# Kernel tuning notes

Hardware: AMD Instinct MI355X
Metric: run time of the kernel (lower is better)

## Reference

```python
import jax, jax.numpy as jnp
import numpy as np

N_TASK, N_WORKER, N_STATION = 20000, 5000, 1000
D, HEADS, LAYERS = 64, 4, 2
EDGE_COUNTS = [50000, 30000, 30000, 40000, 40000]
# (n_src, n_dst) per relation: precedes, assigned_to, has_task, can_do, done_by
EDGE_SPEC = [(N_TASK, N_TASK), (N_TASK, N_STATION), (N_STATION, N_TASK), (N_WORKER, N_TASK), (N_TASK, N_WORKER)]
EDGE_TYPES = [('task', 'task'), ('task', 'station'), ('station', 'task'), ('worker', 'task'), ('task', 'worker')]


def setup_inputs() -> dict:
    key = jax.random.key(0)
    ks = iter(jax.random.split(key, 64))
    inp = {}
    inp['x_task'] = jax.random.normal(next(ks), (N_TASK, 16), jnp.float32)
    inp['x_worker'] = jax.random.normal(next(ks), (N_WORKER, 12), jnp.float32)
    inp['x_station'] = jax.random.normal(next(ks), (N_STATION, 10), jnp.float32)
    for i, (E, (ns, nd)) in enumerate(zip(EDGE_COUNTS, EDGE_SPEC)):
        src = jax.random.randint(next(ks), (E,), 0, ns)
        dst = jax.random.randint(next(ks), (E,), 0, nd)
        inp[f'ei{i}'] = jnp.stack([src, dst]).astype(jnp.int32)
    def lin(k, i, o):
        return jax.random.normal(k, (i, o), jnp.float32) / np.float32(np.sqrt(i))
    # feature embedder params (Linear + LayerNorm affine) per node type
    for name, fd in [('task', 16), ('worker', 12), ('station', 10)]:
        inp[f'W_{name}'] = lin(next(ks), fd, D)
        inp[f'b_{name}'] = jnp.zeros((D,), jnp.float32)
        inp[f'g_{name}'] = jnp.ones((D,), jnp.float32)
        inp[f'beta_{name}'] = jnp.zeros((D,), jnp.float32)
    # stacked GATv2 params: [layers, 5 edge types, ...]
    inp['gat_Wl'] = jax.random.normal(next(ks), (LAYERS, 5, D, HEADS * D), jnp.float32) / np.float32(np.sqrt(D))
    inp['gat_Wr'] = jax.random.normal(next(ks), (LAYERS, 5, D, HEADS * D), jnp.float32) / np.float32(np.sqrt(D))
    inp['gat_att'] = jax.random.normal(next(ks), (LAYERS, 5, HEADS, D), jnp.float32) * np.float32(0.1)
    inp['gat_bias'] = jnp.zeros((LAYERS, 5, D), jnp.float32)
    return inp


def _layer_norm(x, g, b):
    m = x.mean(-1, keepdims=True)
    v = ((x - m) ** 2).mean(-1, keepdims=True)
    return (x - m) * jax.lax.rsqrt(v + 1e-5) * g + b


def _gatv2(x_src, x_dst, ei, Wl, Wr, att, bias):
    # GATv2Conv, concat=False (mean over heads), no self loops
    n_dst = x_dst.shape[0]
    xl = (x_src @ Wl).reshape(-1, HEADS, D)  # [Ns,H,Dh]
    xr = (x_dst @ Wr).reshape(-1, HEADS, D)  # [Nd,H,Dh]
    src, dst = ei[0], ei[1]
    e = jax.nn.leaky_relu(xl[src] + xr[dst], 0.2)          # [E,H,Dh]
    logits = jnp.einsum('ehd,hd->eh', e, att)              # [E,H]
    m = jax.ops.segment_max(logits, dst, num_segments=n_dst)
    ex = jnp.exp(logits - m[dst])
    denom = jax.ops.segment_sum(ex, dst, num_segments=n_dst)
    alpha = ex / denom[dst]                                # segment softmax per dst node
    out = jax.ops.segment_sum(alpha[..., None] * xl[src], dst, num_segments=n_dst)
    return out.mean(axis=1) + bias                         # [Nd,D]


def _forward(x_task, x_worker, x_station, eis,
             W_task, b_task, g_task, beta_task,
             W_worker, b_worker, g_worker, beta_worker,
             W_station, b_station, g_station, beta_station,
             gat_Wl, gat_Wr, gat_att, gat_bias):
    x = {
        'task': jax.nn.relu(_layer_norm(x_task @ W_task + b_task, g_task, beta_task)),
        'worker': jax.nn.relu(_layer_norm(x_worker @ W_worker + b_worker, g_worker, beta_worker)),
        'station': jax.nn.relu(_layer_norm(x_station @ W_station + b_station, g_station, beta_station)),
    }
    for l in range(LAYERS):
        agg = {'task': 0.0, 'worker': 0.0, 'station': 0.0}
        for t, (st, dt) in enumerate(EDGE_TYPES):
            agg[dt] = agg[dt] + _gatv2(x[st], x[dt], eis[t], gat_Wl[l, t], gat_Wr[l, t], gat_att[l, t], gat_bias[l, t])
        x = {k: jax.nn.relu(agg[k]) + x[k] for k in x}  # HeteroConv sum aggr, then ReLU + residual
    gc = jnp.concatenate([
        x['station'].mean(0), x['task'].mean(0), x['worker'].mean(0),
        x['station'].max(0), x['task'].max(0), x['worker'].max(0),
    ])[None, :]  # [1, 6*D]
    return x['task'], x['worker'], x['station'], gc


def reference(x_task, x_worker, x_station, ei0, ei1, ei2, ei3, ei4,
              W_task, b_task, g_task, beta_task,
              W_worker, b_worker, g_worker, beta_worker,
              W_station, b_station, g_station, beta_station,
              gat_Wl, gat_Wr, gat_att, gat_bias):
    return _forward(x_task, x_worker, x_station, (ei0, ei1, ei2, ei3, ei4),
                    W_task, b_task, g_task, beta_task,
                    W_worker, b_worker, g_worker, beta_worker,
                    W_station, b_station, g_station, beta_station,
                    gat_Wl, gat_Wr, gat_att, gat_bias)
```

## Files before the change

kernel.cpp:

```cpp
#include <hip/hip_runtime.h>
#include <math.h>

#define NT 20000
#define NW 5000
#define NS 1000

typedef __attribute__((ext_vector_type(8))) short bf16x8;
typedef __attribute__((ext_vector_type(4))) float f32x4;

struct GemmSeg { const short* X; const short* Wt; short* Y; int N; int blk0; };
struct GemmTab { GemmSeg s[10]; int nseg; };

struct GatSeg { const int* rowp; const int* col; const short* xl; const short* xr;
                const float* att; const float* bias; float* agg; int Nd; int wave0; };
struct GatTab { GatSeg s[5]; int nseg; };

struct EdgeSeg { const int* ei; int* cnt; int* col; int E; int blk0; };
struct EdgeTab { EdgeSeg s[5]; int nseg; };

struct ScanTab { int* cnt[5]; int* rowp[5]; int n[5]; };

__device__ __forceinline__ float wsum64(float v) {
  #pragma unroll
  for (int o = 32; o > 0; o >>= 1) v += __shfl_xor(v, o, 64);
  return v;
}
__device__ __forceinline__ short f2b(float f) {
  unsigned u = __float_as_uint(f);
  unsigned r = (u + 0x7FFFu + ((u >> 16) & 1u)) >> 16;
  return (short)(unsigned short)r;
}
__device__ __forceinline__ float blo(unsigned x) { return __uint_as_float(x << 16); }
__device__ __forceinline__ float bhi(unsigned x) { return __uint_as_float(x & 0xFFFF0000u); }

__global__ void wprep_kernel(const float* __restrict__ gWl, const float* __restrict__ gWr,
                             short* __restrict__ Wlt, short* __restrict__ Wrt) {
  int idx = blockIdx.x * 256 + threadIdx.x;
  int side = idx >= 163840;
  int j = idx - side * 163840;
  int m = j >> 14;
  int e = j & 16383;
  int k = e >> 8, colv = e & 255;
  const float* src = side ? gWr : gWl;
  short* dst = side ? Wrt : Wlt;
  dst[m * 16384 + colv * 64 + k] = f2b(src[m * 16384 + e]);
}

__global__ void embed_kernel(const float* __restrict__ x, const float* __restrict__ W,
                             const float* __restrict__ b, const float* __restrict__ g,
                             const float* __restrict__ beta, float* __restrict__ y,
                             short* __restrict__ yb, int N, int FD) {
  int gid  = blockIdx.x * blockDim.x + threadIdx.x;
  int wid  = gid >> 6;
  int lane = gid & 63;
  if (wid >= N) return;
  const float* xr = x + (size_t)wid * FD;
  float acc = b[lane];
  for (int k = 0; k < FD; ++k) acc = fmaf(xr[k], W[k * 64 + lane], acc);
  float m = wsum64(acc) * (1.f / 64.f);
  float d = acc - m;
  float v = wsum64(d * d) * (1.f / 64.f);
  float o = d * rsqrtf(v + 1e-5f) * g[lane] + beta[lane];
  o = fmaxf(o, 0.f);
  y[(size_t)wid * 64 + lane] = o;
  yb[(size_t)wid * 64 + lane] = f2b(o);
}

__global__ void zero_kernel(unsigned int* __restrict__ p, long long n) {
  long long i  = (long long)blockIdx.x * blockDim.x + threadIdx.x;
  long long st = (long long)gridDim.x * blockDim.x;
  for (; i < n; i += st) p[i] = 0u;
}

__global__ void count_kernel(EdgeTab tab) {
  int b = blockIdx.x, si = 0;
  for (int i = 1; i < tab.nseg; ++i) if (b >= tab.s[i].blk0) si = i;
  EdgeSeg sg = tab.s[si];
  int e = (b - sg.blk0) * 256 + threadIdx.x;
  if (e < sg.E) atomicAdd(&sg.cnt[sg.ei[sg.E + e]], 1);
}

__global__ void scan_kernel(ScanTab tab) {
  int t = blockIdx.x;
  int* cnt = tab.cnt[t]; int* rowp = tab.rowp[t]; int n = tab.n[t];
  __shared__ int wsums[16];
  __shared__ int carry_s;
  int tid = threadIdx.x, lane = tid & 63, w = tid >> 6;
  if (tid == 0) carry_s = 0;
  __syncthreads();
  for (int base = 0; base < n; base += 1024) {
    int i = base + tid;
    int v = (i < n) ? cnt[i] : 0;
    int s = v;
    #pragma unroll
    for (int o = 1; o < 64; o <<= 1) { int x = __shfl_up(s, o, 64); if (lane >= o) s += x; }
    if (lane == 63) wsums[w] = s;
    __syncthreads();
    if (w == 0 && lane < 16) {
      int x = wsums[lane];
      #pragma unroll
      for (int o = 1; o < 16; o <<= 1) { int y = __shfl_up(x, o, 16); if (lane >= o) x += y; }
      wsums[lane] = x;
    }
    __syncthreads();
    int carry   = carry_s;
    int waveoff = (w == 0) ? 0 : wsums[w - 1];
    int exc     = carry + waveoff + s - v;
    if (i < n) { rowp[i] = exc; cnt[i] = exc; }
    __syncthreads();
    if (tid == 0) carry_s += wsums[15];
    __syncthreads();
  }
  if (threadIdx.x == 0) rowp[n] = carry_s;
}

__global__ void fill_kernel(EdgeTab tab) {
  int b = blockIdx.x, si = 0;
  for (int i = 1; i < tab.nseg; ++i) if (b >= tab.s[i].blk0) si = i;
  EdgeSeg sg = tab.s[si];
  int e = (b - sg.blk0) * 256 + threadIdx.x;
  if (e >= sg.E) return;
  int s = sg.ei[e], d = sg.ei[sg.E + e];
  int pos = atomicAdd(&sg.cnt[d], 1);
  sg.col[pos] = s;
}

__global__ __launch_bounds__(256) void gemm_kernel(GemmTab tab) {
  __shared__ short lds[4096 + 16384];
  int b = blockIdx.x, si = 0;
  for (int i = 1; i < tab.nseg; ++i) if (b >= tab.s[i].blk0) si = i;
  GemmSeg sg = tab.s[si];
  int r0 = (b - sg.blk0) * 64;
  int tid = threadIdx.x;
  #pragma unroll
  for (int it = 0; it < 2; ++it) {
    int idx = it * 256 + tid;
    int row = idx >> 3, kq = idx & 7;
    bf16x8 v = {0, 0, 0, 0, 0, 0, 0, 0};
    if (r0 + row < sg.N) v = *(const bf16x8*)&sg.X[(size_t)(r0 + row) * 64 + kq * 8];
    *(bf16x8*)&lds[(row * 8 + (kq ^ (row & 7))) * 8] = v;
  }
  #pragma unroll
  for (int it = 0; it < 8; ++it) {
    int idx = it * 256 + tid;
    int col = idx >> 3, kq = idx & 7;
    bf16x8 v = *(const bf16x8*)&sg.Wt[col * 64 + kq * 8];
    *(bf16x8*)&lds[4096 + (col * 8 + (kq ^ (col & 7))) * 8] = v;
  }
  __syncthreads();
  int lane = tid & 63, wv = tid >> 6;
  int r = lane & 15, hk = lane >> 4;
  f32x4 acc[4][4];
  #pragma unroll
  for (int rt = 0; rt < 4; ++rt)
    #pragma unroll
    for (int ct = 0; ct < 4; ++ct) acc[rt][ct] = (f32x4){0.f, 0.f, 0.f, 0.f};
  #pragma unroll
  for (int kk = 0; kk < 2; ++kk) {
    int kq = kk * 4 + hk;
    bf16x8 a[4], bb[4];
    #pragma unroll
    for (int rt = 0; rt < 4; ++rt) {
      int row = rt * 16 + r;
      a[rt] = *(const bf16x8*)&lds[(row * 8 + (kq ^ (row & 7))) * 8];
    }
    #pragma unroll
    for (int ct = 0; ct < 4; ++ct) {
      int col = wv * 64 + ct * 16 + r;
      bb[ct] = *(const bf16x8*)&lds[4096 + (col * 8 + (kq ^ (col & 7))) * 8];
    }
    #pragma unroll
    for (int rt = 0; rt < 4; ++rt)
      #pragma unroll
      for (int ct = 0; ct < 4; ++ct)
        acc[rt][ct] = __builtin_amdgcn_mfma_f32_16x16x32_bf16(a[rt], bb[ct], acc[rt][ct], 0, 0, 0);
  }
  #pragma unroll
  for (int rt = 0; rt < 4; ++rt) {
    #pragma unroll
    for (int j = 0; j < 4; ++j) {
      int row = r0 + rt * 16 + hk * 4 + j;
      if (row < sg.N) {
        #pragma unroll
        for (int ct = 0; ct < 4; ++ct) {
          int col = wv * 64 + ct * 16 + r;
          sg.Y[(size_t)row * 256 + col] = f2b(acc[rt][ct][j]);
        }
      }
    }
  }
}

__global__ void gat_kernel(GatTab tab) {
  int gwave = (blockIdx.x * blockDim.x + threadIdx.x) >> 6;
  int lane  = threadIdx.x & 63;
  int si = 0;
  for (int i = 1; i < tab.nseg; ++i) if (gwave >= tab.s[i].wave0) si = i;
  GatSeg sg = tab.s[si];
  int n = gwave - sg.wave0;
  if (n >= sg.Nd) return;
  int h = lane >> 4, lig = lane & 15;
  int beg = sg.rowp[n], end = sg.rowp[n + 1];
  uint2 xru = *(const uint2*)&sg.xr[(size_t)n * 256 + h * 64 + lig * 4];
  float xr0 = blo(xru.x), xr1 = bhi(xru.x), xr2 = blo(xru.y), xr3 = bhi(xru.y);
  float4 a4 = *(const float4*)&sg.att[h * 64 + lig * 4];
  float den = 0.f, c0 = 0.f, c1 = 0.f, c2 = 0.f, c3 = 0.f;
  if (end > beg) {
    int sNxt = sg.col[beg];
    uint2 w = *(const uint2*)&sg.xl[(size_t)sNxt * 256 + h * 64 + lig * 4];
    if (beg + 1 < end) sNxt = sg.col[beg + 1];
    for (int i = beg; i < end; ++i) {
      uint2 wc = w;
      if (i + 1 < end)
        w = *(const uint2*)&sg.xl[(size_t)sNxt * 256 + h * 64 + lig * 4];
      if (i + 2 < end) sNxt = sg.col[i + 2];
      float f0 = blo(wc.x), f1 = bhi(wc.x), f2v = blo(wc.y), f3 = bhi(wc.y);
      float vx = f0 + xr0, vy = f1 + xr1, vz = f2v + xr2, vw = f3 + xr3;
      vx = fmaxf(vx, 0.2f * vx); vy = fmaxf(vy, 0.2f * vy);
      vz = fmaxf(vz, 0.2f * vz); vw = fmaxf(vw, 0.2f * vw);
      float d = fmaf(vx, a4.x, fmaf(vy, a4.y, fmaf(vz, a4.z, vw * a4.w)));
      d += __shfl_xor(d, 1, 64);
      d += __shfl_xor(d, 2, 64);
      d += __shfl_xor(d, 4, 64);
      d += __shfl_xor(d, 8, 64);
      float e = __expf(d);
      den += e;
      c0 = fmaf(e, f0, c0); c1 = fmaf(e, f1, c1);
      c2 = fmaf(e, f2v, c2); c3 = fmaf(e, f3, c3);
    }
  }
  float4 o = make_float4(0.f, 0.f, 0.f, 0.f);
  if (end > beg) {
    float inv = 1.f / den;
    o.x = c0 * inv; o.y = c1 * inv; o.z = c2 * inv; o.w = c3 * inv;
  }
  o.x += __shfl_xor(o.x, 16, 64); o.x += __shfl_xor(o.x, 32, 64);
  o.y += __shfl_xor(o.y, 16, 64); o.y += __shfl_xor(o.y, 32, 64);
  o.z += __shfl_xor(o.z, 16, 64); o.z += __shfl_xor(o.z, 32, 64);
  o.w += __shfl_xor(o.w, 16, 64); o.w += __shfl_xor(o.w, 32, 64);
  if (lane < 16) {
    float4 b4 = *(const float4*)&sg.bias[lane * 4];
    float4 res;
    res.x = fmaf(0.25f, o.x, b4.x); res.y = fmaf(0.25f, o.y, b4.y);
    res.z = fmaf(0.25f, o.z, b4.z); res.w = fmaf(0.25f, o.w, b4.w);
    *(float4*)&sg.agg[(size_t)n * 64 + lane * 4] = res;
  }
}

__global__ void combine_kernel(const float* __restrict__ aT0, const float* __restrict__ aT2,
                               const float* __restrict__ aT3, const float* __restrict__ aW,
                               const float* __restrict__ aS,
                               const float* __restrict__ xT, const float* __restrict__ xW,
                               const float* __restrict__ xS,
                               float* __restrict__ oT, float* __restrict__ oW,
                               float* __restrict__ oS,
                               short* __restrict__ bT, short* __restrict__ bW,
                               short* __restrict__ bS) {
  int i = blockIdx.x * 256 + threadIdx.x;
  const int nT = NT * 64, nW = NW * 64, nS = NS * 64;
  if (i < nT) {
    float v = fmaxf(aT0[i] + aT2[i] + aT3[i], 0.f) + xT[i];
    oT[i] = v; if (bT) bT[i] = f2b(v);
  } else if (i < nT + nW) {
    int j = i - nT;
    float v = fmaxf(aW[j], 0.f) + xW[j];
    oW[j] = v; if (bW) bW[j] = f2b(v);
  } else if (i < nT + nW + nS) {
    int j = i - nT - nW;
    float v = fmaxf(aS[j], 0.f) + xS[j];
    oS[j] = v; if (bS) bS[j] = f2b(v);
  }
}

__global__ __launch_bounds__(256) void pool1_kernel(const float* __restrict__ xt,
                                                    const float* __restrict__ xw,
                                                    const float* __restrict__ xs,
                                                    float* __restrict__ part_sum,
                                                    float* __restrict__ part_max) {
  int b = blockIdx.x;
  const float* x; int N, base, nb;
  if (b < 80)       { x = xt; N = NT; base = 0;   nb = 80; }
  else if (b < 100) { x = xw; N = NW; base = 80;  nb = 20; }
  else              { x = xs; N = NS; base = 100; nb = 4;  }
  int local = b - base;
  int lane = threadIdx.x & 63, w = threadIdx.x >> 6;
  int waveIdx = local * 4 + w, stride = nb * 4;
  float s = 0.f, mx = -3e38f;
  for (int r = waveIdx; r < N; r += stride) {
    float v = x[(size_t)r * 64 + lane];
    s += v; mx = fmaxf(mx, v);
  }
  __shared__ float ss[4][64], sm[4][64];
  ss[w][lane] = s; sm[w][lane] = mx;
  __syncthreads();
  if (w == 0) {
    #pragma unroll
    for (int i = 1; i < 4; ++i) { s += ss[i][lane]; mx = fmaxf(mx, sm[i][lane]); }
    part_sum[(size_t)b * 64 + lane] = s;
    part_max[(size_t)b * 64 + lane] = mx;
  }
}

__global__ void pool2_kernel(const float* __restrict__ part_sum,
                             const float* __restrict__ part_max,
                             float* __restrict__ gc) {
  int b = blockIdx.x;
  int lane = threadIdx.x & 63, w = threadIdx.x >> 6;
  int off, cnt, N, mi;
  if (b == 0)      { off = 100; cnt = 4;  N = NS; mi = 0;   }
  else if (b == 1) { off = 0;   cnt = 80; N = NT; mi = 64;  }
  else             { off = 80;  cnt = 20; N = NW; mi = 128; }
  float s = 0.f, mx = -3e38f;
  for (int i = w; i < cnt; i += 4) {
    s += part_sum[(size_t)(off + i) * 64 + lane];
    mx = fmaxf(mx, part_max[(size_t)(off + i) * 64 + lane]);
  }
  __shared__ float ss[4][64], sm[4][64];
  ss[w][lane] = s; sm[w][lane] = mx;
  __syncthreads();
  if (w == 0) {
    #pragma unroll
    for (int i = 1; i < 4; ++i) { s += ss[i][lane]; mx = fmaxf(mx, sm[i][lane]); }
    gc[mi + lane] = s / (float)N;
    gc[192 + mi + lane] = mx;
  }
}

extern "C" void kernel_launch(void* const* d_in, const int* in_sizes, int n_in,
                              void* d_out, int out_size, void* d_ws, size_t ws_size,
                              hipStream_t stream) {
  const float* x_in[3] = {(const float*)d_in[0], (const float*)d_in[1], (const float*)d_in[2]};
  const int*   ei[5]   = {(const int*)d_in[3], (const int*)d_in[4], (const int*)d_in[5],
                          (const int*)d_in[6], (const int*)d_in[7]};
  const float* Wemb[3] = {(const float*)d_in[8],  (const float*)d_in[12], (const float*)d_in[16]};
  const float* bemb[3] = {(const float*)d_in[9],  (const float*)d_in[13], (const float*)d_in[17]};
  const float* gemb[3] = {(const float*)d_in[10], (const float*)d_in[14], (const float*)d_in[18]};
  const float* beemb[3]= {(const float*)d_in[11], (const float*)d_in[15], (const float*)d_in[19]};
  const float* gWl   = (const float*)d_in[20];
  const float* gWr   = (const float*)d_in[21];
  const float* gatt  = (const float*)d_in[22];
  const float* gbias = (const float*)d_in[23];

  const int NN[3]  = {NT, NW, NS};
  const int FD[3]  = {16, 12, 10};
  const int EC[5]  = {50000, 30000, 30000, 40000, 40000};
  const int STy[5] = {0, 0, 2, 1, 0};
  const int DTy[5] = {0, 2, 0, 0, 1};

  char* p = (char*)d_ws;
  auto alloc = [&](size_t bytes) -> void* {
    void* r = (void*)p;
    p += (bytes + 255) & ~(size_t)255;
    return r;
  };
  float* xc[3];  short* xcb[3];
  for (int k = 0; k < 3; ++k) xc[k]  = (float*)alloc((size_t)NN[k] * 64 * 4);
  for (int k = 0; k < 3; ++k) xcb[k] = (short*)alloc((size_t)NN[k] * 64 * 2);
  float* aggT0 = (float*)alloc((size_t)NT * 64 * 4);
  float* aggS  = (float*)alloc((size_t)NS * 64 * 4);
  float* aggT2 = (float*)alloc((size_t)NT * 64 * 4);
  float* aggT3 = (float*)alloc((size_t)NT * 64 * 4);
  float* aggW  = (float*)alloc((size_t)NW * 64 * 4);
  float* aggOf[5] = {aggT0, aggS, aggT2, aggT3, aggW};
  int* nxtAll = (int*)alloc((size_t)66000 * 4);
  int  nxtOff[5] = {0, NT, NT + NS, 2 * NT + NS, 3 * NT + NS};
  int* nxt[5]; for (int t = 0; t < 5; ++t) nxt[t] = nxtAll + nxtOff[t];
  int *rowp[5], *col[5];
  for (int t = 0; t < 5; ++t) {
    rowp[t] = (int*)alloc((size_t)(NN[DTy[t]] + 1) * 4);
    col[t]  = (int*)alloc((size_t)EC[t] * 4);
  }
  float* psum = (float*)alloc((size_t)104 * 64 * 4);
  float* pmax = (float*)alloc((size_t)104 * 64 * 4);
  short* Wlt  = (short*)alloc((size_t)10 * 16384 * 2);
  short* Wrt  = (short*)alloc((size_t)10 * 16384 * 2);

  size_t used = (size_t)(p - (char*)d_ws);
  size_t fusedExtra = (size_t)132000 * 256 * 2 + (1 << 20);
  bool fused = (ws_size - used) >= fusedExtra;
  short *xlT[5], *xrT[5];
  if (fused) {
    for (int t = 0; t < 5; ++t) {
      xlT[t] = (short*)alloc((size_t)NN[STy[t]] * 256 * 2);
      xrT[t] = (short*)alloc((size_t)NN[DTy[t]] * 256 * 2);
    }
  } else {
    short* xlb = (short*)alloc((size_t)NT * 256 * 2);
    short* xrb = (short*)alloc((size_t)NT * 256 * 2);
    for (int t = 0; t < 5; ++t) { xlT[t] = xlb; xrT[t] = xrb; }
  }

  wprep_kernel<<<1280, 256, 0, stream>>>(gWl, gWr, Wlt, Wrt);

  for (int k = 0; k < 3; ++k) {
    int threads = NN[k] * 64;
    embed_kernel<<<(threads + 255) / 256, 256, 0, stream>>>(
        x_in[k], Wemb[k], bemb[k], gemb[k], beemb[k], xc[k], xcb[k], NN[k], FD[k]);
  }

  zero_kernel<<<64, 256, 0, stream>>>((unsigned*)nxtAll, 66000);
  EdgeTab etab; etab.nseg = 5;
  int eb = 0;
  for (int t = 0; t < 5; ++t) {
    etab.s[t] = {ei[t], nxt[t], col[t], EC[t], eb};
    eb += (EC[t] + 255) / 256;
  }
  count_kernel<<<eb, 256, 0, stream>>>(etab);
  ScanTab stab;
  for (int t = 0; t < 5; ++t) { stab.cnt[t] = nxt[t]; stab.rowp[t] = rowp[t]; stab.n[t] = NN[DTy[t]]; }
  scan_kernel<<<5, 1024, 0, stream>>>(stab);
  fill_kernel<<<eb, 256, 0, stream>>>(etab);

  float* outT = (float*)d_out;
  float* outW = outT + (size_t)NT * 64;
  float* outS = outW + (size_t)NW * 64;
  float* gc   = outS + (size_t)NS * 64;

  for (int l = 0; l < 2; ++l) {
    if (fused) {
      GemmTab gt; gt.nseg = 10;
      int gb = 0;
      for (int t = 0; t < 5; ++t) {
        size_t off = (size_t)(l * 5 + t);
        gt.s[2 * t + 0] = {xcb[STy[t]], Wlt + off * 16384, xlT[t], NN[STy[t]], gb};
        gb += (NN[STy[t]] + 63) / 64;
        gt.s[2 * t + 1] = {xcb[DTy[t]], Wrt + off * 16384, xrT[t], NN[DTy[t]], gb};
        gb += (NN[DTy[t]] + 63) / 64;
      }
      gemm_kernel<<<gb, 256, 0, stream>>>(gt);

      GatTab at; at.nseg = 5;
      int wv = 0;
      for (int t = 0; t < 5; ++t) {
        size_t off = (size_t)(l * 5 + t);
        at.s[t] = {rowp[t], col[t], xlT[t], xrT[t], gatt + off * 256, gbias + off * 64,
                   aggOf[t], NN[DTy[t]], wv};
        wv += NN[DTy[t]];
      }
      gat_kernel<<<(wv * 64 + 255) / 256, 256, 0, stream>>>(at);
    } else {
      for (int t = 0; t < 5; ++t) {
        size_t off = (size_t)(l * 5 + t);
        GemmTab gt; gt.nseg = 2;
        gt.s[0] = {xcb[STy[t]], Wlt + off * 16384, xlT[t], NN[STy[t]], 0};
        int gb = (NN[STy[t]] + 63) / 64;
        gt.s[1] = {xcb[DTy[t]], Wrt + off * 16384, xrT[t], NN[DTy[t]], gb};
        gb += (NN[DTy[t]] + 63) / 64;
        gemm_kernel<<<gb, 256, 0, stream>>>(gt);
        GatTab at; at.nseg = 1;
        at.s[0] = {rowp[t], col[t], xlT[t], xrT[t], gatt + off * 256, gbias + off * 64,
                   aggOf[t], NN[DTy[t]], 0};
        gat_kernel<<<((NN[DTy[t]] + 3) / 4), 256, 0, stream>>>(at);
      }
    }
    float* dT = (l == 1) ? outT : xc[0];
    float* dW = (l == 1) ? outW : xc[1];
    float* dS = (l == 1) ? outS : xc[2];
    short* bT = (l == 1) ? nullptr : xcb[0];
    short* bW = (l == 1) ? nullptr : xcb[1];
    short* bS = (l == 1) ? nullptr : xcb[2];
    combine_kernel<<<(26000 * 64 + 255) / 256, 256, 0, stream>>>(
        aggT0, aggT2, aggT3, aggW, aggS, xc[0], xc[1], xc[2], dT, dW, dS, bT, bW, bS);
  }

  pool1_kernel<<<104, 256, 0, stream>>>(outT, outW, outS, psum, pmax);
  pool2_kernel<<<3, 256, 0, stream>>>(psum, pmax, gc);
}
```

Baseline: 240.5 us.

## Merge setup kernels, stage GEMM output via LDS, batch GAT gathers, vectorize combine

Folds the zeroing of the edge counters into the weight-prep kernel and merges the three per-type embed launches into one, using a packed parameter buffer. The GEMM epilogue now stages bf16 results in padded LDS so it can write 16-byte coalesced rows instead of scattered 2-byte stores. The GAT kernel loads up to 64 neighbour indices per wave and issues 8 neighbour feature loads at once, giving more memory-level parallelism than the old one-ahead prefetch. The combine kernel is switched to float4 loads and packed bf16 stores. Together these cut launch count and memory transactions, at the cost of an extra tiny pack kernel, two added barriers in the GEMM, and higher register use in the GAT kernel.

Result: slower. 253.9 us (+5.6%).

```diff
diff --git a/kernel.cpp b/kernel.cpp
--- a/kernel.cpp
+++ b/kernel.cpp
@@ -34,8 +34,10 @@
 __device__ __forceinline__ float bhi(unsigned x) { return __uint_as_float(x & 0xFFFF0000u); }
 
 __global__ void wprep_kernel(const float* __restrict__ gWl, const float* __restrict__ gWr,
-                             short* __restrict__ Wlt, short* __restrict__ Wrt) {
+                             short* __restrict__ Wlt, short* __restrict__ Wrt,
+                             int* __restrict__ nxtAll, int nZero) {
   int idx = blockIdx.x * 256 + threadIdx.x;
+  if (idx < nZero) nxtAll[idx] = 0;
   int side = idx >= 163840;
   int j = idx - side * 163840;
   int m = j >> 14;
@@ -46,30 +48,44 @@
   dst[m * 16384 + colv * 64 + k] = f2b(src[m * 16384 + e]);
 }
 
-__global__ void embed_kernel(const float* __restrict__ x, const float* __restrict__ W,
-                             const float* __restrict__ b, const float* __restrict__ g,
-                             const float* __restrict__ beta, float* __restrict__ y,
-                             short* __restrict__ yb, int N, int FD) {
+__global__ void embed_kernel(const float* __restrict__ xT, const float* __restrict__ xW,
+                             const float* __restrict__ xS,
+                             const float* __restrict__ WT, const float* __restrict__ WW,
+                             const float* __restrict__ WS,
+                             const float* __restrict__ pT, const float* __restrict__ pW,
+                             const float* __restrict__ pS,
+                             float* __restrict__ yT, float* __restrict__ yW,
+                             float* __restrict__ yS,
+                             short* __restrict__ bT, short* __restrict__ bW,
+                             short* __restrict__ bS) {
   int gid  = blockIdx.x * blockDim.x + threadIdx.x;
   int wid  = gid >> 6;
   int lane = gid & 63;
-  if (wid >= N) return;
-  const float* xr = x + (size_t)wid * FD;
-  float acc = b[lane];
+  const float* x; const float* W; const float* pp; float* y; short* yb; int FD; int n;
+  if (wid < NT)            { x = xT; W = WT; pp = pT; y = yT; yb = bT; FD = 16; n = wid; }
+  else if (wid < NT + NW)  { x = xW; W = WW; pp = pW; y = yW; yb = bW; FD = 12; n = wid - NT; }
+  else if (wid < NT + NW + NS) { x = xS; W = WS; pp = pS; y = yS; yb = bS; FD = 10; n = wid - NT - NW; }
+  else return;
+  const float* xr = x + (size_t)n * FD;
+  float acc = pp[lane];
   for (int k = 0; k < FD; ++k) acc = fmaf(xr[k], W[k * 64 + lane], acc);
   float m = wsum64(acc) * (1.f / 64.f);
   float d = acc - m;
   float v = wsum64(d * d) * (1.f / 64.f);
-  float o = d * rsqrtf(v + 1e-5f) * g[lane] + beta[lane];
+  float o = d * rsqrtf(v + 1e-5f) * pp[64 + lane] + pp[128 + lane];
   o = fmaxf(o, 0.f);
-  y[(size_t)wid * 64 + lane] = o;
-  yb[(size_t)wid * 64 + lane] = f2b(o);
-}
-
-__global__ void zero_kernel(unsigned int* __restrict__ p, long long n) {
-  long long i  = (long long)blockIdx.x * blockDim.x + threadIdx.x;
-  long long st = (long long)gridDim.x * blockDim.x;
-  for (; i < n; i += st) p[i] = 0u;
+  y[(size_t)n * 64 + lane] = o;
+  yb[(size_t)n * 64 + lane] = f2b(o);
+}
+
+__global__ void packp_kernel(const float* b0, const float* g0, const float* be0,
+                             const float* b1, const float* g1, const float* be1,
+                             const float* b2, const float* g2, const float* be2,
+                             float* __restrict__ out) {
+  int i = threadIdx.x;
+  out[i]       = b0[i];  out[64 + i]  = g0[i];  out[128 + i] = be0[i];
+  out[192 + i] = b1[i];  out[256 + i] = g1[i];  out[320 + i] = be1[i];
+  out[384 + i] = b2[i];  out[448 + i] = g2[i];  out[512 + i] = be2[i];
 }
 
 __global__ void count_kernel(EdgeTab tab) {
@@ -126,7 +142,7 @@
 }
 
 __global__ __launch_bounds__(256) void gemm_kernel(GemmTab tab) {
-  __shared__ short lds[4096 + 16384];
+  __shared__ short lds[4096 + 16896];
   int b = blockIdx.x, si = 0;
   for (int i = 1; i < tab.nseg; ++i) if (b >= tab.s[i].blk0) si = i;
   GemmSeg sg = tab.s[si];
@@ -175,18 +191,24 @@
       for (int ct = 0; ct < 4; ++ct)
         acc[rt][ct] = __builtin_amdgcn_mfma_f32_16x16x32_bf16(a[rt], bb[ct], acc[rt][ct], 0, 0, 0);
   }
-  #pragma unroll
-  for (int rt = 0; rt < 4; ++rt) {
+  __syncthreads();
+  #pragma unroll
+  for (int rt = 0; rt < 4; ++rt)
     #pragma unroll
     for (int j = 0; j < 4; ++j) {
-      int row = r0 + rt * 16 + hk * 4 + j;
-      if (row < sg.N) {
-        #pragma unroll
-        for (int ct = 0; ct < 4; ++ct) {
-          int col = wv * 64 + ct * 16 + r;
-          sg.Y[(size_t)row * 256 + col] = f2b(acc[rt][ct][j]);
-        }
-      }
+      int rowl = rt * 16 + hk * 4 + j;
+      #pragma unroll
+      for (int ct = 0; ct < 4; ++ct)
+        lds[rowl * 264 + wv * 64 + ct * 16 + r] = f2b(acc[rt][ct][j]);
+    }
+  __syncthreads();
+  #pragma unroll
+  for (int it = 0; it < 8; ++it) {
+    int idx = it * 256 + tid;
+    int row = idx >> 5, v8 = idx & 31;
+    if (r0 + row < sg.N) {
+      bf16x8 v = *(const bf16x8*)&lds[row * 264 + v8 * 8];
+      *(bf16x8*)&sg.Y[(size_t)(r0 + row) * 256 + v8 * 8] = v;
     }
   }
 }
@@ -200,37 +222,45 @@
   int n = gwave - sg.wave0;
   if (n >= sg.Nd) return;
   int h = lane >> 4, lig = lane & 15;
+  uint2 xru = *(const uint2*)&sg.xr[(size_t)n * 256 + h * 64 + lig * 4];
+  float4 a4 = *(const float4*)&sg.att[h * 64 + lig * 4];
   int beg = sg.rowp[n], end = sg.rowp[n + 1];
-  uint2 xru = *(const uint2*)&sg.xr[(size_t)n * 256 + h * 64 + lig * 4];
+  int d = end - beg;
   float xr0 = blo(xru.x), xr1 = bhi(xru.x), xr2 = blo(xru.y), xr3 = bhi(xru.y);
-  float4 a4 = *(const float4*)&sg.att[h * 64 + lig * 4];
   float den = 0.f, c0 = 0.f, c1 = 0.f, c2 = 0.f, c3 = 0.f;
-  if (end > beg) {
-    int sNxt = sg.col[beg];
-    uint2 w = *(const uint2*)&sg.xl[(size_t)sNxt * 256 + h * 64 + lig * 4];
-    if (beg + 1 < end) sNxt = sg.col[beg + 1];
-    for (int i = beg; i < end; ++i) {
-      uint2 wc = w;
-      if (i + 1 < end)
-        w = *(const uint2*)&sg.xl[(size_t)sNxt * 256 + h * 64 + lig * 4];
-      if (i + 2 < end) sNxt = sg.col[i + 2];
-      float f0 = blo(wc.x), f1 = bhi(wc.x), f2v = blo(wc.y), f3 = bhi(wc.y);
-      float vx = f0 + xr0, vy = f1 + xr1, vz = f2v + xr2, vw = f3 + xr3;
-      vx = fmaxf(vx, 0.2f * vx); vy = fmaxf(vy, 0.2f * vy);
-      vz = fmaxf(vz, 0.2f * vz); vw = fmaxf(vw, 0.2f * vw);
-      float d = fmaf(vx, a4.x, fmaf(vy, a4.y, fmaf(vz, a4.z, vw * a4.w)));
-      d += __shfl_xor(d, 1, 64);
-      d += __shfl_xor(d, 2, 64);
-      d += __shfl_xor(d, 4, 64);
-      d += __shfl_xor(d, 8, 64);
-      float e = __expf(d);
-      den += e;
-      c0 = fmaf(e, f0, c0); c1 = fmaf(e, f1, c1);
-      c2 = fmaf(e, f2v, c2); c3 = fmaf(e, f3, c3);
+  for (int sc = 0; sc < d; sc += 64) {
+    int scn = min(64, d - sc);
+    int myc = (lane < scn) ? sg.col[beg + sc + lane] : 0;
+    for (int cb = 0; cb < scn; cb += 8) {
+      int m = min(8, scn - cb);
+      uint2 w[8];
+      #pragma unroll
+      for (int k = 0; k < 8; ++k)
+        if (k < m) {
+          int c = __shfl(myc, cb + k, 64);
+          w[k] = *(const uint2*)&sg.xl[(size_t)c * 256 + h * 64 + lig * 4];
+        }
+      #pragma unroll
+      for (int k = 0; k < 8; ++k)
+        if (k < m) {
+          float f0 = blo(w[k].x), f1 = bhi(w[k].x), f2v = blo(w[k].y), f3 = bhi(w[k].y);
+          float vx = f0 + xr0, vy = f1 + xr1, vz = f2v + xr2, vw = f3 + xr3;
+          vx = fmaxf(vx, 0.2f * vx); vy = fmaxf(vy, 0.2f * vy);
+          vz = fmaxf(vz, 0.2f * vz); vw = fmaxf(vw, 0.2f * vw);
+          float dd = fmaf(vx, a4.x, fmaf(vy, a4.y, fmaf(vz, a4.z, vw * a4.w)));
+          dd += __shfl_xor(dd, 1, 64);
+          dd += __shfl_xor(dd, 2, 64);
+          dd += __shfl_xor(dd, 4, 64);
+          dd += __shfl_xor(dd, 8, 64);
+          float e = __expf(dd);
+          den += e;
+          c0 = fmaf(e, f0, c0); c1 = fmaf(e, f1, c1);
+          c2 = fmaf(e, f2v, c2); c3 = fmaf(e, f3, c3);
+        }
     }
   }
   float4 o = make_float4(0.f, 0.f, 0.f, 0.f);
-  if (end > beg) {
+  if (d > 0) {
     float inv = 1.f / den;
     o.x = c0 * inv; o.y = c1 * inv; o.z = c2 * inv; o.w = c3 * inv;
   }
@@ -247,28 +277,37 @@
   }
 }
 
-__global__ void combine_kernel(const float* __restrict__ aT0, const float* __restrict__ aT2,
-                               const float* __restrict__ aT3, const float* __restrict__ aW,
-                               const float* __restrict__ aS,
-                               const float* __restrict__ xT, const float* __restrict__ xW,
-                               const float* __restrict__ xS,
-                               float* __restrict__ oT, float* __restrict__ oW,
-                               float* __restrict__ oS,
-                               short* __restrict__ bT, short* __restrict__ bW,
-                               short* __restrict__ bS) {
+__global__ void combine_kernel(const float4* __restrict__ aT0, const float4* __restrict__ aT2,
+                               const float4* __restrict__ aT3, const float4* __restrict__ aW,
+                               const float4* __restrict__ aS,
+                               const float4* __restrict__ xT, const float4* __restrict__ xW,
+                               const float4* __restrict__ xS,
+                               float4* __restrict__ oT, float4* __restrict__ oW,
+                               float4* __restrict__ oS,
+                               unsigned* __restrict__ bT, unsigned* __restrict__ bW,
+                               unsigned* __restrict__ bS) {
   int i = blockIdx.x * 256 + threadIdx.x;
-  const int nT = NT * 64, nW = NW * 64, nS = NS * 64;
-  if (i < nT) {
-    float v = fmaxf(aT0[i] + aT2[i] + aT3[i], 0.f) + xT[i];
-    oT[i] = v; if (bT) bT[i] = f2b(v);
-  } else if (i < nT + nW) {
-    int j = i - nT;
-    float v = fmaxf(aW[j], 0.f) + xW[j];
-    oW[j] = v; if (bW) bW[j] = f2b(v);
-  } else if (i < nT + nW + nS) {
-    int j = i - nT - nW;
-    float v = fmaxf(aS[j], 0.f) + xS[j];
-    oS[j] = v; if (bS) bS[j] = f2b(v);
+  const int nT4 = NT * 16, nW4 = NW * 16, nS4 = NS * 16;
+  const float4* a; const float4* x; float4* o; unsigned* bo; int j; bool sum3 = false;
+  const float4 *a2 = nullptr, *a3 = nullptr;
+  if (i < nT4)                 { a = aT0; a2 = aT2; a3 = aT3; x = xT; o = oT; bo = bT; j = i; sum3 = true; }
+  else if (i < nT4 + nW4)      { a = aW; x = xW; o = oW; bo = bW; j = i - nT4; }
+  else if (i < nT4 + nW4 + nS4){ a = aS; x = xS; o = oS; bo = bS; j = i - nT4 - nW4; }
+  else return;
+  float4 av = a[j];
+  if (sum3) {
+    float4 v2 = a2[j], v3 = a3[j];
+    av.x += v2.x + v3.x; av.y += v2.y + v3.y; av.z += v2.z + v3.z; av.w += v2.w + v3.w;
+  }
+  float4 xv = x[j];
+  float4 r;
+  r.x = fmaxf(av.x, 0.f) + xv.x; r.y = fmaxf(av.y, 0.f) + xv.y;
+  r.z = fmaxf(av.z, 0.f) + xv.z; r.w = fmaxf(av.w, 0.f) + xv.w;
+  o[j] = r;
+  if (bo) {
+    unsigned lo = (unsigned)(unsigned short)f2b(r.x) | ((unsigned)(unsigned short)f2b(r.y) << 16);
+    unsigned hi = (unsigned)(unsigned short)f2b(r.z) | ((unsigned)(unsigned short)f2b(r.w) << 16);
+    bo[j * 2] = lo; bo[j * 2 + 1] = hi;
   }
 }
 
@@ -342,7 +381,6 @@
   const float* gbias = (const float*)d_in[23];
 
   const int NN[3]  = {NT, NW, NS};
-  const int FD[3]  = {16, 12, 10};
   const int EC[5]  = {50000, 30000, 30000, 40000, 40000};
   const int STy[5] = {0, 0, 2, 1, 0};
   const int DTy[5] = {0, 2, 0, 0, 1};
@@ -374,6 +412,7 @@
   float* pmax = (float*)alloc((size_t)104 * 64 * 4);
   short* Wlt  = (short*)alloc((size_t)10 * 16384 * 2);
   short* Wrt  = (short*)alloc((size_t)10 * 16384 * 2);
+  float* ppk  = (float*)alloc((size_t)576 * 4);
 
   size_t used = (size_t)(p - (char*)d_ws);
   size_t fusedExtra = (size_t)132000 * 256 * 2 + (1 << 20);
@@ -390,15 +429,16 @@
     for (int t = 0; t < 5; ++t) { xlT[t] = xlb; xrT[t] = xrb; }
   }
 
-  wprep_kernel<<<1280, 256, 0, stream>>>(gWl, gWr, Wlt, Wrt);
-
-  for (int k = 0; k < 3; ++k) {
-    int threads = NN[k] * 64;
-    embed_kernel<<<(threads + 255) / 256, 256, 0, stream>>>(
-        x_in[k], Wemb[k], bemb[k], gemb[k], beemb[k], xc[k], xcb[k], NN[k], FD[k]);
-  }
-
-  zero_kernel<<<64, 256, 0, stream>>>((unsigned*)nxtAll, 66000);
+  wprep_kernel<<<1280, 256, 0, stream>>>(gWl, gWr, Wlt, Wrt, nxtAll, 66000);
+  packp_kernel<<<1, 64, 0, stream>>>(bemb[0], gemb[0], beemb[0],
+                                     bemb[1], gemb[1], beemb[1],
+                                     bemb[2], gemb[2], beemb[2], ppk);
+
+  embed_kernel<<<(26000 * 64 + 255) / 256, 256, 0, stream>>>(
+      x_in[0], x_in[1], x_in[2], Wemb[0], Wemb[1], Wemb[2],
+      ppk, ppk + 192, ppk + 384,
+      xc[0], xc[1], xc[2], xcb[0], xcb[1], xcb[2]);
+
   EdgeTab etab; etab.nseg = 5;
   int eb = 0;
   for (int t = 0; t < 5; ++t) {
@@ -456,11 +496,14 @@
     float* dT = (l == 1) ? outT : xc[0];
     float* dW = (l == 1) ? outW : xc[1];
     float* dS = (l == 1) ? outS : xc[2];
-    short* bT = (l == 1) ? nullptr : xcb[0];
-    short* bW = (l == 1) ? nullptr : xcb[1];
-    short* bS = (l == 1) ? nullptr : xcb[2];
-    combine_kernel<<<(26000 * 64 + 255) / 256, 256, 0, stream>>>(
-        aggT0, aggT2, aggT3, aggW, aggS, xc[0], xc[1], xc[2], dT, dW, dS, bT, bW, bS);
+    unsigned* bT = (l == 1) ? nullptr : (unsigned*)xcb[0];
+    unsigned* bW = (l == 1) ? nullptr : (unsigned*)xcb[1];
+    unsigned* bS = (l == 1) ? nullptr : (unsigned*)xcb[2];
+    combine_kernel<<<(26000 * 16 + 255) / 256, 256, 0, stream>>>(
+        (const float4*)aggT0, (const float4*)aggT2, (const float4*)aggT3,
+        (const float4*)aggW, (const float4*)aggS,
+        (const float4*)xc[0], (const float4*)xc[1], (const float4*)xc[2],
+        (float4*)dT, (float4*)dW, (float4*)dS, bT, bW, bS);
   }
 
   pool1_kernel<<<104, 256, 0, stream>>>(outT, outW, outS, psum, pmax);
```
